# Performance work log

Hardware: AMD Instinct MI355X
Metric: run time of the kernel (lower is better)

Reference implementation:

```python
import jax, jax.numpy as jnp
import numpy as np
import math

EPS = 1e-6          # eps for safe cumprod / clamping
CHUNK = 4           # chunk_size w
SHARP = 1.0         # sharpening_factor
NOISE_STD = 1.0
N_HEADS = 4
ADIM = 512


def moving_sum(x, back, forward):
    """Windowed running sum over last axis: out[k] = sum_{j=k-back}^{k+forward} x[j].
    Equivalent to the conv1d trick in the original (all-ones filter)."""
    k = x.shape[-1]
    pad = [(0, 0)] * (x.ndim - 1) + [(back, forward)]
    c = jnp.cumsum(jnp.pad(x, pad), axis=-1)
    c0 = jnp.concatenate([jnp.zeros_like(c[..., :1]), c], axis=-1)
    w = back + forward
    return c0[..., w + 1: w + 1 + k] - c0[..., :k]


def setup_inputs() -> dict:
    rng = jax.random.key(0)
    ks = jax.random.split(rng, 12)
    B, qlen, klen, kdim, qdim, adim = 8, 256, 2048, 512, 512, ADIM
    s = 0.02
    return {
        "key_enc": jax.random.normal(ks[0], (B, klen, kdim), jnp.float32),
        "query":   jax.random.normal(ks[1], (B, qlen, qdim), jnp.float32),
        "noise":   jax.random.normal(ks[2], (B, qlen, klen), jnp.float32),
        # monotonic energy params
        "Wk_m": jax.random.normal(ks[3], (kdim, adim), jnp.float32) * s,
        "bk_m": jnp.zeros((adim,), jnp.float32),
        "Wq_m": jax.random.normal(ks[4], (qdim, adim), jnp.float32) * s,
        "bq_m": jnp.zeros((adim,), jnp.float32),
        "r":    jnp.array([-4.0], jnp.float32),
        # chunkwise energy params (multi-head)
        "Wk_c": jax.random.normal(ks[5], (kdim, adim), jnp.float32) * s,
        "bk_c": jnp.zeros((adim,), jnp.float32),
        "Wq_c": jax.random.normal(ks[6], (qdim, adim), jnp.float32) * s,
        "bq_c": jnp.zeros((adim,), jnp.float32),
    }


def _mocha_beta(key_enc, query, noise, Wk_m, bk_m, Wq_m, bq_m, r,
                Wk_c, bk_c, Wq_c, bq_c):
    B, klen, _ = key_enc.shape
    qlen = query.shape[1]
    H = N_HEADS
    dk = ADIM // H
    scale = math.sqrt(ADIM)

    # --- monotonic energy (single head): [B, qlen, klen]
    k_m = key_enc @ Wk_m + bk_m
    q_m = query @ Wq_m + bq_m
    e_mono = jnp.einsum('bqa,bka->bqk', q_m, k_m) / scale + r[0]

    # --- p_choose with additive gaussian noise (encourages discreteness)
    p_choose = jax.nn.sigmoid(e_mono + noise * NOISE_STD)  # [B,q,k]

    # --- safe cumprod of (1 - p) via exclusive cumsum in log space
    log1mp = jnp.log(jnp.clip(1.0 - p_choose, EPS, 1.0))
    cumprod_1mp = jnp.exp(jnp.cumsum(log1mp, axis=-1) - log1mp)  # exclusive

    # --- monotonic alpha recurrence over query steps (parallel-mode MoChA)
    aw0 = jnp.zeros((B, klen), jnp.float32).at[:, 0].set(1.0)

    def step(aw_prev, inp):
        p_i, cp_i = inp  # [B, klen]
        alpha_i = p_i * cp_i * jnp.cumsum(
            aw_prev / jnp.clip(cp_i, EPS, 1.0), axis=-1)
        return alpha_i, alpha_i

    xs = (jnp.swapaxes(p_choose, 0, 1), jnp.swapaxes(cumprod_1mp, 0, 1))
    _, alpha_q = jax.lax.scan(step, aw0, xs)          # [q, B, k]
    alpha = jnp.swapaxes(alpha_q, 0, 1)                # [B, q, k]

    # --- chunkwise energy (multi-head): [B, H, q, k]
    k_c = (key_enc @ Wk_c + bk_c).reshape(B, klen, H, dk)
    q_c = (query @ Wq_c + bq_c).reshape(B, qlen, H, dk)
    e_chunk = jnp.einsum('bqhd,bkhd->bhqk', q_c, k_c) / scale

    # --- efficient chunkwise attention (clipped-logit moving-sum softmax)
    e = e_chunk - jnp.max(e_chunk, axis=3, keepdims=True)
    softmax_exp = jnp.maximum(jnp.exp(e), 1e-5)
    denom = moving_sum(softmax_exp, back=CHUNK - 1, forward=0)
    beta = softmax_exp * moving_sum(
        alpha[:, None] * SHARP / denom, back=0, forward=CHUNK - 1)
    return beta  # [B, H, q, k]


def reference(key_enc, query, noise, Wk_m, bk_m, Wq_m, bq_m, r,
              Wk_c, bk_c, Wq_c, bq_c):
    return _mocha_beta(key_enc, query, noise, Wk_m, bk_m, Wq_m, bq_m, r,
                       Wk_c, bk_c, Wq_c, bq_c)
```

## Files before the change

kernel.cpp:

```cpp
#include <hip/hip_runtime.h>
#include <math.h>

#define BATCH   8
#define QLEN    256
#define KLEN    2048
#define KDIM    512
#define NHEADS  4
#define DKH     128
#define NG      5
#define QROWS   (BATCH * QLEN)
#define GCOLS   (NG * 512)

static constexpr float INV_SCALE = 0.04419417382415922f;
static constexpr float EPSV = 1e-6f;

typedef __attribute__((ext_vector_type(8))) short bf16x8;
typedef __attribute__((ext_vector_type(4))) float f32x4;

__device__ __forceinline__ unsigned short f2bf(float f) {
    unsigned u = __builtin_bit_cast(unsigned, f);
    u += 0x7fffu + ((u >> 16) & 1u);
    return (unsigned short)(u >> 16);
}
__device__ __forceinline__ float bf2f(unsigned short u) {
    unsigned x = (unsigned)u << 16;
    return __builtin_bit_cast(float, x);
}

__device__ __forceinline__ void lds_barrier() {
    __asm__ volatile("s_waitcnt lgkmcnt(0)\n\ts_barrier" ::: "memory");
}

__device__ __forceinline__ void gload_lds16(const void* g, void* l) {
    __builtin_amdgcn_global_load_lds(
        (const __attribute__((address_space(1))) void*)g,
        (__attribute__((address_space(3))) void*)l, 16, 0, 0);
}

#define NKXB 8192
#define NQXB 1024
__global__ __launch_bounds__(256) void prep(
    const float* __restrict__ key_enc, const float* __restrict__ query,
    const float* __restrict__ Wk_m, const float* __restrict__ Wk_c,
    const float* __restrict__ Wq_m, const float* __restrict__ Wq_c,
    unsigned short* __restrict__ kx, unsigned short* __restrict__ qx,
    unsigned short* __restrict__ kwm, unsigned short* __restrict__ kwc,
    unsigned short* __restrict__ qwm, unsigned short* __restrict__ qwc)
{
    const int gb = blockIdx.x, tid = threadIdx.x;
    const float* x; unsigned short* y; int i;
    if (gb < NKXB)              { x = key_enc; y = kx; i = gb * 256 + tid; }
    else if (gb < NKXB + NQXB)  { x = query;   y = qx; i = (gb - NKXB) * 256 + tid; }
    else {
        const int w = gb - NKXB - NQXB;
        const int which = w >> 8;
        i = (w & 255) * 256 + tid;
        x = (which == 0) ? Wk_m : (which == 1) ? Wk_c : (which == 2) ? Wq_m : Wq_c;
        y = (which == 0) ? kwm  : (which == 1) ? kwc  : (which == 2) ? qwm  : qwc;
    }
    float4 v = ((const float4*)x)[i];
    ushort4 o;
    o.x = f2bf(v.x); o.y = f2bf(v.y); o.z = f2bf(v.z); o.w = f2bf(v.w);
    ((ushort4*)y)[i] = o;
}

__device__ __forceinline__ void mfma_nt_staged(
    const unsigned short* __restrict__ A, const unsigned short* __restrict__ B,
    int lda, int ldb, int bm, int bn,
    unsigned short* AsLDS, unsigned short* BsLDS, f32x4 acc[4][4], int ksteps)
{
    const int t = threadIdx.x;
    const int wv = t >> 6, ln = t & 63;
    const int r = ln & 15, quad = ln >> 4;
    const int wm = (wv >> 1) * 64, wn = (wv & 1) * 64;
    const int srow = wv * 16 + (ln >> 2);
    const int scol = (ln & 3) * 8;

    for (int ks = 0; ks < ksteps; ++ks) {
        const int k0 = ks * 32;
        #pragma unroll
        for (int j = 0; j < 2; ++j) {
            gload_lds16(A + (size_t)(bm + j * 64 + srow) * lda + k0 + scol,
                        AsLDS + (size_t)(j * 64 + wv * 16) * 32);
            gload_lds16(B + (size_t)(bn + j * 64 + srow) * ldb + k0 + scol,
                        BsLDS + (size_t)(j * 64 + wv * 16) * 32);
        }
        __syncthreads();
        bf16x8 af[4], bg[4];
        #pragma unroll
        for (int f = 0; f < 4; ++f)
            af[f] = *(const bf16x8*)(AsLDS + (size_t)(wm + f * 16 + r) * 32 + quad * 8);
        #pragma unroll
        for (int f = 0; f < 4; ++f)
            bg[f] = *(const bf16x8*)(BsLDS + (size_t)(wn + f * 16 + r) * 32 + quad * 8);
        #pragma unroll
        for (int i = 0; i < 4; ++i)
            #pragma unroll
            for (int j2 = 0; j2 < 4; ++j2)
                acc[i][j2] = __builtin_amdgcn_mfma_f32_16x16x32_bf16(
                    af[i], bg[j2], acc[i][j2], 0, 0, 0);
        __syncthreads();
    }
}

__device__ __forceinline__ void zero_acc(f32x4 acc[4][4]) {
    #pragma unroll
    for (int i = 0; i < 4; ++i)
        #pragma unroll
        for (int j = 0; j < 4; ++j)
            acc[i][j] = f32x4{0.f, 0.f, 0.f, 0.f};
}

__global__ __launch_bounds__(256) void smallg(
    const unsigned short* __restrict__ kwm, const unsigned short* __restrict__ kwc,
    const unsigned short* __restrict__ qwm, const unsigned short* __restrict__ qwc,
    const float* __restrict__ Wk_mf, const float* __restrict__ Wk_cf,
    const float* __restrict__ Wq_mf,
    const float* __restrict__ bq_m, const float* __restrict__ bk_m,
    const float* __restrict__ bq_c,
    unsigned short* __restrict__ GT, float* __restrict__ aux)
{
    __shared__ unsigned short As[128 * 32];
    __shared__ unsigned short Bs[128 * 32];
    __shared__ float red[256];
    const int blk = blockIdx.x, tid = threadIdx.x;

    if (blk < 80) {
        const int seg = blk >> 4, t = blk & 15;
        const int bm = (t >> 2) * 128, bn = (t & 3) * 128;
        const unsigned short *A, *B; int ks;
        if (seg == 0) { A = kwm; B = qwm; ks = 16; }
        else { const int h = seg - 1; A = kwc + h * 128; B = qwc + h * 128; ks = 4; }
        f32x4 acc[4][4]; zero_acc(acc);
        mfma_nt_staged(A, B, 512, 512, bm, bn, As, Bs, acc, ks);
        const int wv = tid >> 6, ln = tid & 63;
        const int r = ln & 15, quad = ln >> 4;
        const int m0 = bm + (wv >> 1) * 64, n0 = bn + (wv & 1) * 64;
        #pragma unroll
        for (int j = 0; j < 4; ++j) {
            const int n = n0 + j * 16 + r;
            #pragma unroll
            for (int i = 0; i < 4; ++i)
                #pragma unroll
                for (int reg = 0; reg < 4; ++reg) {
                    const int m = m0 + i * 16 + quad * 4 + reg;
                    GT[(size_t)(seg * 512 + m) * 512 + n] = f2bf(acc[i][j][reg]);
                }
        }
        return;
    }
    const int ab = blk - 80;
    if (ab < 2) {
        const int d = ab * 256 + tid;
        const float* row = Wk_mf + (size_t)d * 512;
        float s = 0.f;
        for (int j = 0; j < 512; j += 4) {
            float4 a = *(const float4*)(row + j);
            float4 b = *(const float4*)(bq_m + j);
            s += a.x * b.x + a.y * b.y + a.z * b.z + a.w * b.w;
        }
        aux[d] = s; return;
    }
    if (ab < 10) {
        const int t = ab - 2, h = t >> 1;
        const int d = (t & 1) * 256 + tid;
        const float* row = Wk_cf + (size_t)d * 512 + h * 128;
        const float* bv = bq_c + h * 128;
        float s = 0.f;
        for (int j = 0; j < 128; j += 4) {
            float4 a = *(const float4*)(row + j);
            float4 b = *(const float4*)(bv + j);
            s += a.x * b.x + a.y * b.y + a.z * b.z + a.w * b.w;
        }
        aux[512 + h * 512 + d] = s; return;
    }
    if (ab < 12) {
        const int d = (ab - 10) * 256 + tid;
        const float* row = Wq_mf + (size_t)d * 512;
        float s = 0.f;
        for (int j = 0; j < 512; j += 4) {
            float4 a = *(const float4*)(row + j);
            float4 b = *(const float4*)(bk_m + j);
            s += a.x * b.x + a.y * b.y + a.z * b.z + a.w * b.w;
        }
        aux[GCOLS + d] = s; return;
    }
    float s = bq_m[tid] * bk_m[tid] + bq_m[tid + 256] * bk_m[tid + 256];
    red[tid] = s; __syncthreads();
    for (int o = 128; o > 0; o >>= 1) {
        if (tid < o) red[tid] += red[tid + o];
        __syncthreads();
    }
    if (tid == 0) aux[GCOLS + 512] = red[0];
}

__global__ __launch_bounds__(256) void qg_kernel(
    const unsigned short* __restrict__ qx, const unsigned short* __restrict__ GT,
    const float* __restrict__ aux,
    unsigned short* __restrict__ qg, float* __restrict__ vq2)
{
    __shared__ unsigned short As[128 * 32];
    __shared__ unsigned short Bs[128 * 32];
    __shared__ float wuS[512];
    const int v = blockIdx.x, tid = threadIdx.x;
    if (v < 320) {
        const int by = v / 20, bx = v % 20;
        const int bm = by * 128, bn = bx * 128;
        f32x4 acc[4][4]; zero_acc(acc);
        mfma_nt_staged(qx, GT, 512, 512, bm, bn, As, Bs, acc, 16);
        const int wv = tid >> 6, ln = tid & 63;
        const int r = ln & 15, quad = ln >> 4;
        const int m0 = bm + (wv >> 1) * 64, n0 = bn + (wv & 1) * 64;
        #pragma unroll
        for (int j = 0; j < 4; ++j) {
            const int n = n0 + j * 16 + r;
            const float wvb = aux[n];
            #pragma unroll
            for (int i = 0; i < 4; ++i)
                #pragma unroll
                for (int reg = 0; reg < 4; ++reg) {
                    const int m = m0 + i * 16 + quad * 4 + reg;
                    qg[(size_t)m * GCOLS + n] = f2bf(acc[i][j][reg] + wvb);
                }
        }
        return;
    }
    wuS[tid] = aux[GCOLS + tid];
    wuS[tid + 256] = aux[GCOLS + tid + 256];
    __syncthreads();
    const float cc = aux[GCOLS + 512];
    const int q = (v - 320) * 256 + tid;
    const unsigned short* row = qx + (size_t)q * 512;
    float s = 0.f;
    for (int j = 0; j < 512; j += 4) {
        ushort4 a = *(const ushort4*)(row + j);
        s = fmaf(bf2f(a.x), wuS[j], s);
        s = fmaf(bf2f(a.y), wuS[j + 1], s);
        s = fmaf(bf2f(a.z), wuS[j + 2], s);
        s = fmaf(bf2f(a.w), wuS[j + 3], s);
    }
    vq2[q] = (s + cc) * INV_SCALE;
}

__global__ __launch_bounds__(256) void pchoose_mfma(
    const unsigned short* __restrict__ qg, const unsigned short* __restrict__ kx,
    const float* __restrict__ noise, const float* __restrict__ rp,
    const float* __restrict__ vq2, float* __restrict__ p)
{
    __shared__ unsigned short As[128 * 32];
    __shared__ unsigned short Bs[128 * 32];
    const int b = blockIdx.z;
    const unsigned short* A = qg + (size_t)b * QLEN * GCOLS;
    const unsigned short* B = kx + (size_t)b * KLEN * 512;
    const int bm = blockIdx.y * 128, bn = blockIdx.x * 128;
    f32x4 acc[4][4]; zero_acc(acc);
    mfma_nt_staged(A, B, GCOLS, 512, bm, bn, As, Bs, acc, 16);
    const int wv = threadIdx.x >> 6, ln = threadIdx.x & 63;
    const int r = ln & 15, quad = ln >> 4;
    const int m0 = bm + (wv >> 1) * 64, n0 = bn + (wv & 1) * 64;
    const float rv = rp[0];
    #pragma unroll
    for (int i = 0; i < 4; ++i) {
        #pragma unroll
        for (int reg = 0; reg < 4; ++reg) {
            const int q = m0 + i * 16 + quad * 4 + reg;
            const size_t rowoff = ((size_t)b * QLEN + q) * KLEN;
            const float vq = vq2[b * QLEN + q] + rv;
            #pragma unroll
            for (int j = 0; j < 4; ++j) {
                const int k = n0 + j * 16 + r;
                const float e = acc[i][j][reg] * INV_SCALE + vq + noise[rowoff + k];
                p[rowoff + k] = __builtin_amdgcn_rcpf(1.0f + __expf(-e));
            }
        }
    }
}

__device__ __forceinline__ float wave_incl_scan(float x)
{
#define DPP_ADD(ctrl, rmask, bctrl)                                            \
    { int _t = __builtin_amdgcn_update_dpp(0, __builtin_bit_cast(int, x),      \
                                           ctrl, rmask, 0xf, bctrl);           \
      x += __builtin_bit_cast(float, _t); }
    DPP_ADD(0x111, 0xf, true)
    DPP_ADD(0x112, 0xf, true)
    DPP_ADD(0x114, 0xf, true)
    DPP_ADD(0x118, 0xf, true)
    DPP_ADD(0x142, 0xa, false)
    DPP_ADD(0x143, 0xc, false)
#undef DPP_ADD
    return x;
}

__device__ __forceinline__ float row_prefix8(float x)
{
#define DPP_ADD(ctrl)                                                          \
    { int _t = __builtin_amdgcn_update_dpp(0, __builtin_bit_cast(int, x),      \
                                           ctrl, 0xf, 0xf, true);              \
      x += __builtin_bit_cast(float, _t); }
    DPP_ADD(0x111)
    DPP_ADD(0x112)
    DPP_ADD(0x114)
#undef DPP_ADD
    return x;
}

__global__ __launch_bounds__(256) void cumprod_mr(
    const float* __restrict__ p, float* __restrict__ mArr, float* __restrict__ rArr)
{
    const size_t row = blockIdx.x;
    const float* pr = p + row * KLEN;
    float* mr = mArr + row * KLEN;
    float* rr = rArr + row * KLEN;
    const int tid = threadIdx.x;
    const int lane = tid & 63, wid = tid >> 6;
    __shared__ float waveTot[4];

    float4 v0 = *(const float4*)(pr + tid * 8);
    float4 v1 = *(const float4*)(pr + tid * 8 + 4);
    float pv[8] = {v0.x, v0.y, v0.z, v0.w, v1.x, v1.y, v1.z, v1.w};
    float excl[8];
    float run = 0.0f;
    #pragma unroll
    for (int j = 0; j < 8; ++j) {
        float l = __logf(fminf(fmaxf(1.0f - pv[j], EPSV), 1.0f));
        excl[j] = run;
        run += l;
    }
    float s = wave_incl_scan(run);
    if (lane == 63) waveTot[wid] = s;
    __syncthreads();
    float wex = 0.0f;
    for (int w = 0; w < wid; ++w) wex += waveTot[w];
    const float texcl = wex + s - run;

    float mv[8], rv[8];
    #pragma unroll
    for (int j = 0; j < 8; ++j) {
        const float cpv = __expf(texcl + excl[j]);
        mv[j] = pv[j] * cpv;
        rv[j] = __builtin_amdgcn_rcpf(fminf(fmaxf(cpv, EPSV), 1.0f));
    }
    *(float4*)(mr + tid * 8)     = *(float4*)&mv[0];
    *(float4*)(mr + tid * 8 + 4) = *(float4*)&mv[4];
    *(float4*)(rr + tid * 8)     = *(float4*)&rv[0];
    *(float4*)(rr + tid * 8 + 4) = *(float4*)&rv[4];
}

__global__ __launch_bounds__(512, 1) void alpha_echunk(
    const float* __restrict__ mArr, const float* __restrict__ rArr,
    float* __restrict__ alpha,
    const unsigned short* __restrict__ qg, const unsigned short* __restrict__ kx,
    float* __restrict__ out)
{
    __shared__ __align__(16) char smem[98304];
    const int bid = blockIdx.x;
    const int tid = threadIdx.x;

    if (bid < BATCH) {
        __builtin_amdgcn_s_setprio(1);
        float* slots = (float*)smem;
        const int lane = tid & 63, wid = tid >> 6;
        const float* mrow = mArr + (size_t)bid * QLEN * KLEN + tid * 4;
        const float* rrow = rArr + (size_t)bid * QLEN * KLEN + tid * 4;
        float* arow = alpha + (size_t)bid * QLEN * KLEN + tid * 4;

        float aw0 = 0.f, aw1 = 0.f, aw2 = 0.f, aw3 = 0.f;
        if (tid == 0) aw0 = 1.0f;

        float4 mP0 = *(const float4*)(mrow);
        float4 rP0 = *(const float4*)(rrow);
        float4 mP1 = *(const float4*)(mrow + KLEN);
        float4 rP1 = *(const float4*)(rrow + KLEN);
        float4 mQ0 = *(const float4*)(mrow + 2 * (size_t)KLEN);
        float4 rQ0 = *(const float4*)(rrow + 2 * (size_t)KLEN);
        float4 mQ1 = *(const float4*)(mrow + 3 * (size_t)KLEN);
        float4 rQ1 = *(const float4*)(rrow + 3 * (size_t)KLEN);

#define APAIR(I, M0, R0, M1, R1)                                               \
    {                                                                          \
        const int i_ = (I);                               \
        float4 mc0 = M0, rc0 = R0, mc1 = M1, rc1 = R1;                         \
        const int rn_ = (i_ + 4 < QLEN) ? (i_ + 4) : (QLEN - 2);               \
        M0 = *(const float4*)(mrow + (size_t)rn_ * KLEN);                      \
        R0 = *(const float4*)(rrow + (size_t)rn_ * KLEN);                      \
        M1 = *(const float4*)(mrow + (size_t)(rn_ + 1) * KLEN);               \
        R1 = *(const float4*)(rrow + (size_t)(rn_ + 1) * KLEN);               \
                                 \
        float run = 0.f, i0, i1, i2, i3;                                       \
        run = fmaf(aw0, rc0.x, run); i0 = run;                                 \
        run = fmaf(aw1, rc0.y, run); i1 = run;                                 \
        run = fmaf(aw2, rc0.z, run); i2 = run;                                 \
        run = fmaf(aw3, rc0.w, run); i3 = run;                                 \
        const float sx = wave_incl_scan(run);                                  \
        const float wb = sx - run;                                             \
        const float W0 = wb + i0, W1 = wb + i1, W2 = wb + i2, W3 = wb + i3;    \
                      \
        const float u0 = mc0.x * rc1.x, u1 = mc0.y * rc1.y;                    \
        const float u2 = mc0.z * rc1.z, u3 = mc0.w * rc1.w;                    \
        float ur = u0;       const float U0 = ur;                              \
        ur += u1;            const float U1 = ur;                              \
        ur += u2;            const float U2 = ur;                              \
        ur += u3;            const float U3 = ur;                              \
        const float sU = wave_incl_scan(ur);                                   \
        const float ub = sU - ur;                                              \
        float vr = u0 * W0;              const float V0 = vr;                  \
        vr = fmaf(u1, W1, vr);           const float V1 = vr;                  \
        vr = fmaf(u2, W2, vr);           const float V2 = vr;                  \
        vr = fmaf(u3, W3, vr);           const float V3 = vr;                  \
        const float sV = wave_incl_scan(vr);                                   \
        const float vb = sV - vr;                                              \
        const int par = (i_ >> 1) & 1;                                         \
        if (lane == 63) {                                                      \
            float4 tv; tv.x = sx; tv.y = sU; tv.z = sV; tv.w = 0.f;            \
            *(float4*)(slots + (par * 8 + wid) * 4) = tv;                      \
        }                                                                      \
        lds_barrier();                                                         \
        float4 tr = *(const float4*)(slots + (par * 8 + (lane & 7)) * 4);      \
        const float pT = row_prefix8(tr.x);                                    \
        const float Cex = pT - tr.x;                                           \
        const float t2 = fmaf(Cex, tr.y, tr.z);                                \
        const float pQ = row_prefix8(t2);                                      \
        const float C2ex = pQ - t2;                                            \
        const float b0 = __shfl(Cex, wid);                                     \
        const float b1 = __shfl(C2ex, wid);                                    \
                                                          \
        float4 o0;                                                             \
        o0.x = mc0.x * (b0 + W0); o0.y = mc0.y * (b0 + W1);                    \
        o0.z = mc0.z * (b0 + W2); o0.w = mc0.w * (b0 + W3);                    \
        *(float4*)(arow + (size_t)i_ * KLEN) = o0;                             \
                                                        \
        const float X0 = fmaf(b0, ub + U0, vb + V0);                           \
        const float X1 = fmaf(b0, ub + U1, vb + V1);                           \
        const float X2 = fmaf(b0, ub + U2, vb + V2);                           \
        const float X3 = fmaf(b0, ub + U3, vb + V3);                           \
        aw0 = mc1.x * (b1 + X0); aw1 = mc1.y * (b1 + X1);                      \
        aw2 = mc1.z * (b1 + X2); aw3 = mc1.w * (b1 + X3);                      \
        float4 o1; o1.x = aw0; o1.y = aw1; o1.z = aw2; o1.w = aw3;             \
        *(float4*)(arow + (size_t)(i_ + 1) * KLEN) = o1;                       \
    }

        for (int io = 0; io < QLEN; io += 4) {
            APAIR(io + 0, mP0, rP0, mP1, rP1)
            APAIR(io + 2, mQ0, rQ0, mQ1, rQ1)
        }
#undef APAIR
        __builtin_amdgcn_s_setprio(0);
        return;
    }

    const int v = bid - BATCH;
    const int z = v >> 4;
    const int rest = v & 15;
    const int by = rest >> 3;
    const int bx = rest & 7;
    const int b = z >> 2, h = z & 3;
    unsigned short* As = (unsigned short*)smem;
    unsigned short* Bs = (unsigned short*)(smem + 8192);
    const unsigned short* A = qg + (size_t)(b * QLEN) * GCOLS + 512 + h * 512;
    const unsigned short* B = kx + (size_t)b * KLEN * 512;
    const int bm = by * 128, bn = bx * 256;

    const int wv8 = tid >> 6, ln = tid & 63;
    const int r = ln & 15, quad = ln >> 4;
    const int wr = wv8 >> 2, wc = wv8 & 3;
    const int srow = tid >> 2;
    const int scol = (ln & 3) * 8;

    f32x4 acc[4][4]; zero_acc(acc);
    for (int ks = 0; ks < 16; ++ks) {
        const int k0 = ks * 32;
        gload_lds16(A + (size_t)(bm + srow) * GCOLS + k0 + scol,
                    As + (size_t)wv8 * 512);
        gload_lds16(B + (size_t)(bn + srow) * 512 + k0 + scol,
                    Bs + (size_t)wv8 * 512);
        gload_lds16(B + (size_t)(bn + 128 + srow) * 512 + k0 + scol,
                    Bs + 4096 + (size_t)wv8 * 512);
        __syncthreads();
        bf16x8 af[4], bg[4];
        #pragma unroll
        for (int f = 0; f < 4; ++f)
            af[f] = *(const bf16x8*)(As + (size_t)(wr * 64 + f * 16 + r) * 32 + quad * 8);
        #pragma unroll
        for (int f = 0; f < 4; ++f)
            bg[f] = *(const bf16x8*)(Bs + (size_t)(wc * 64 + f * 16 + r) * 32 + quad * 8);
        #pragma unroll
        for (int i = 0; i < 4; ++i)
            #pragma unroll
            for (int j2 = 0; j2 < 4; ++j2)
                acc[i][j2] = __builtin_amdgcn_mfma_f32_16x16x32_bf16(
                    af[i], bg[j2], acc[i][j2], 0, 0, 0);
        __syncthreads();
    }
    {
        const int m0 = bm + wr * 64, n0 = bn + wc * 64;
        #pragma unroll
        for (int i = 0; i < 4; ++i) {
            #pragma unroll
            for (int reg = 0; reg < 4; ++reg) {
                const int q = m0 + i * 16 + quad * 4 + reg;
                const size_t rowoff = ((size_t)z * QLEN + q) * KLEN;
                #pragma unroll
                for (int j = 0; j < 4; ++j) {
                    const int k = n0 + j * 16 + r;
                    out[rowoff + k] = acc[i][j][reg] * INV_SCALE;
                }
            }
        }
    }
}

__global__ __launch_bounds__(256) void beta_kernel(
    float* __restrict__ eo, const float* __restrict__ alpha)
{
    __shared__ float sse[KLEN + 3];
    __shared__ float su[KLEN + 3];
    __shared__ float wmax[4];

    const int tid = threadIdx.x;
    const int lane = tid & 63, wid = tid >> 6;
    const int row = blockIdx.x;
    const int q = row & (QLEN - 1);
    const int b = row >> 10;
    float* erow = eo + (size_t)row * KLEN;
    const float* arow = alpha + ((size_t)b * QLEN + q) * KLEN;

    if (tid < 3) { sse[tid] = 0.0f; su[KLEN + tid] = 0.0f; }

    float ev[8];
    float lm = -INFINITY;
    #pragma unroll
    for (int j = 0; j < 8; ++j) {
        const int k = tid + 256 * j;
        ev[j] = erow[k];
        lm = fmaxf(lm, ev[j]);
    }
    #pragma unroll
    for (int off = 32; off > 0; off >>= 1) lm = fmaxf(lm, __shfl_xor(lm, off));
    if (lane == 0) wmax[wid] = lm;
    __syncthreads();
    const float mx = fmaxf(fmaxf(wmax[0], wmax[1]), fmaxf(wmax[2], wmax[3]));

    #pragma unroll
    for (int j = 0; j < 8; ++j) {
        const int k = tid + 256 * j;
        sse[k + 3] = fmaxf(__expf(ev[j] - mx), 1e-5f);
    }
    __syncthreads();

    #pragma unroll
    for (int j = 0; j < 8; ++j) {
        const int k = tid + 256 * j;
        const float denom = sse[k + 3] + sse[k + 2] + sse[k + 1] + sse[k];
        su[k] = arow[k] * __builtin_amdgcn_rcpf(denom);
    }
    __syncthreads();

    #pragma unroll
    for (int j = 0; j < 8; ++j) {
        const int k = tid + 256 * j;
        erow[k] = sse[k + 3] * (su[k] + su[k + 1] + su[k + 2] + su[k + 3]);
    }
}

extern "C" void kernel_launch(void* const* d_in, const int* in_sizes, int n_in,
                              void* d_out, int out_size, void* d_ws, size_t ws_size,
                              hipStream_t stream)
{
    (void)in_sizes; (void)n_in; (void)out_size; (void)ws_size;
    const float* key_enc = (const float*)d_in[0];
    const float* query   = (const float*)d_in[1];
    const float* noise   = (const float*)d_in[2];
    const float* Wk_m    = (const float*)d_in[3];
    const float* bk_m    = (const float*)d_in[4];
    const float* Wq_m    = (const float*)d_in[5];
    const float* bq_m    = (const float*)d_in[6];
    const float* rp      = (const float*)d_in[7];
    const float* Wk_c    = (const float*)d_in[8];
    const float* bk_c    = (const float*)d_in[9];
    const float* Wq_c    = (const float*)d_in[10];
    const float* bq_c    = (const float*)d_in[11];
    float* out = (float*)d_out;
    (void)bk_c;

    char* w = (char*)d_ws;
    unsigned short* kx   = (unsigned short*)w; w += (size_t)BATCH * KLEN * KDIM * 2;
    unsigned short* qx   = (unsigned short*)w; w += (size_t)QROWS * KDIM * 2;
    unsigned short* kwm  = (unsigned short*)w; w += (size_t)512 * 512 * 2;
    unsigned short* kwc  = (unsigned short*)w; w += (size_t)512 * 512 * 2;
    unsigned short* qwm  = (unsigned short*)w; w += (size_t)512 * 512 * 2;
    unsigned short* qwc  = (unsigned short*)w; w += (size_t)512 * 512 * 2;
    unsigned short* GT   = (unsigned short*)w; w += (size_t)GCOLS * 512 * 2;
    unsigned short* qg   = (unsigned short*)w; w += (size_t)QROWS * GCOLS * 2;
    float* aux    = (float*)w; w += 4096 * 4;
    float* vq2    = (float*)w; w += QROWS * 4;
    float* p_alpha = (float*)w; w += (size_t)BATCH * QLEN * KLEN * 4;
    float* mArr    = (float*)w; w += (size_t)BATCH * QLEN * KLEN * 4;
    float* rArr    = (float*)w;

    hipLaunchKernelGGL(prep, dim3(NKXB + NQXB + 1024), dim3(256), 0, stream,
                       key_enc, query, Wk_m, Wk_c, Wq_m, Wq_c,
                       kx, qx, kwm, kwc, qwm, qwc);

    hipLaunchKernelGGL(smallg, dim3(93), dim3(256), 0, stream,
                       kwm, kwc, qwm, qwc, Wk_m, Wk_c, Wq_m,
                       bq_m, bk_m, bq_c, GT, aux);

    hipLaunchKernelGGL(qg_kernel, dim3(328), dim3(256), 0, stream,
                       qx, GT, aux, qg, vq2);

    hipLaunchKernelGGL(pchoose_mfma, dim3(KLEN / 128, QLEN / 128, BATCH), dim3(256), 0, stream,
                       qg, kx, noise, rp, vq2, p_alpha);

    hipLaunchKernelGGL(cumprod_mr, dim3(BATCH * QLEN), dim3(256), 0, stream,
                       p_alpha, mArr, rArr);

    hipLaunchKernelGGL(alpha_echunk, dim3(BATCH + 512), dim3(512), 0, stream,
                       mArr, rArr, p_alpha, qg, kx, out);

    hipLaunchKernelGGL(beta_kernel, dim3(BATCH * NHEADS * QLEN), dim3(256), 0, stream,
                       out, p_alpha);
}
```

Baseline: 279.2 us.

## Fuse cumprod into alpha scan and merge weight prep into GEMM kernel

Removes the separate cumprod_mr kernel. The alpha recurrence kernel now computes the safe cumprod (m and 1/cp) for upcoming rows inline from p, which drops the write and re-read of two full BxQxK float arrays. It also folds the weight bf16 conversion into the small Gram GEMM by converting fp32 on the fly, and merges prep and smallg into a single launch. The cost is more serial work and extra cross-wave reductions inside the latency-bound scan loop.

```diff
diff --git a/kernel.cpp b/kernel.cpp
--- a/kernel.cpp
+++ b/kernel.cpp
@@ -37,33 +37,6 @@
         (__attribute__((address_space(3))) void*)l, 16, 0, 0);
 }
 
-#define NKXB 8192
-#define NQXB 1024
-__global__ __launch_bounds__(256) void prep(
-    const float* __restrict__ key_enc, const float* __restrict__ query,
-    const float* __restrict__ Wk_m, const float* __restrict__ Wk_c,
-    const float* __restrict__ Wq_m, const float* __restrict__ Wq_c,
-    unsigned short* __restrict__ kx, unsigned short* __restrict__ qx,
-    unsigned short* __restrict__ kwm, unsigned short* __restrict__ kwc,
-    unsigned short* __restrict__ qwm, unsigned short* __restrict__ qwc)
-{
-    const int gb = blockIdx.x, tid = threadIdx.x;
-    const float* x; unsigned short* y; int i;
-    if (gb < NKXB)              { x = key_enc; y = kx; i = gb * 256 + tid; }
-    else if (gb < NKXB + NQXB)  { x = query;   y = qx; i = (gb - NKXB) * 256 + tid; }
-    else {
-        const int w = gb - NKXB - NQXB;
-        const int which = w >> 8;
-        i = (w & 255) * 256 + tid;
-        x = (which == 0) ? Wk_m : (which == 1) ? Wk_c : (which == 2) ? Wq_m : Wq_c;
-        y = (which == 0) ? kwm  : (which == 1) ? kwc  : (which == 2) ? qwm  : qwc;
-    }
-    float4 v = ((const float4*)x)[i];
-    ushort4 o;
-    o.x = f2bf(v.x); o.y = f2bf(v.y); o.z = f2bf(v.z); o.w = f2bf(v.w);
-    ((ushort4*)y)[i] = o;
-}
-
 __device__ __forceinline__ void mfma_nt_staged(
     const unsigned short* __restrict__ A, const unsigned short* __restrict__ B,
     int lda, int ldb, int bm, int bn,
@@ -103,6 +76,57 @@
     }
 }
 
+__device__ __forceinline__ void mfma_nt_staged_f32(
+    const float* __restrict__ A, const float* __restrict__ B,
+    int lda, int ldb, int bm, int bn,
+    unsigned short* AsLDS, unsigned short* BsLDS, f32x4 acc[4][4], int ksteps)
+{
+    const int t = threadIdx.x;
+    const int wv = t >> 6, ln = t & 63;
+    const int r = ln & 15, quad = ln >> 4;
+    const int wm = (wv >> 1) * 64, wn = (wv & 1) * 64;
+    const int srow = wv * 16 + (ln >> 2);
+    const int scol = (ln & 3) * 8;
+
+    for (int ks = 0; ks < ksteps; ++ks) {
+        const int k0 = ks * 32;
+        #pragma unroll
+        for (int j = 0; j < 2; ++j) {
+            const float* ap = A + (size_t)(bm + j * 64 + srow) * lda + k0 + scol;
+            float4 a0 = *(const float4*)ap, a1 = *(const float4*)(ap + 4);
+            bf16x8 av;
+            av[0] = (short)f2bf(a0.x); av[1] = (short)f2bf(a0.y);
+            av[2] = (short)f2bf(a0.z); av[3] = (short)f2bf(a0.w);
+            av[4] = (short)f2bf(a1.x); av[5] = (short)f2bf(a1.y);
+            av[6] = (short)f2bf(a1.z); av[7] = (short)f2bf(a1.w);
+            *(bf16x8*)(AsLDS + (size_t)(j * 64 + wv * 16) * 32 + ln * 8) = av;
+            const float* bp = B + (size_t)(bn + j * 64 + srow) * ldb + k0 + scol;
+            float4 b0 = *(const float4*)bp, b1 = *(const float4*)(bp + 4);
+            bf16x8 bv;
+            bv[0] = (short)f2bf(b0.x); bv[1] = (short)f2bf(b0.y);
+            bv[2] = (short)f2bf(b0.z); bv[3] = (short)f2bf(b0.w);
+            bv[4] = (short)f2bf(b1.x); bv[5] = (short)f2bf(b1.y);
+            bv[6] = (short)f2bf(b1.z); bv[7] = (short)f2bf(b1.w);
+            *(bf16x8*)(BsLDS + (size_t)(j * 64 + wv * 16) * 32 + ln * 8) = bv;
+        }
+        __syncthreads();
+        bf16x8 af[4], bg[4];
+        #pragma unroll
+        for (int f = 0; f < 4; ++f)
+            af[f] = *(const bf16x8*)(AsLDS + (size_t)(wm + f * 16 + r) * 32 + quad * 8);
+        #pragma unroll
+        for (int f = 0; f < 4; ++f)
+            bg[f] = *(const bf16x8*)(BsLDS + (size_t)(wn + f * 16 + r) * 32 + quad * 8);
+        #pragma unroll
+        for (int i = 0; i < 4; ++i)
+            #pragma unroll
+            for (int j2 = 0; j2 < 4; ++j2)
+                acc[i][j2] = __builtin_amdgcn_mfma_f32_16x16x32_bf16(
+                    af[i], bg[j2], acc[i][j2], 0, 0, 0);
+        __syncthreads();
+    }
+}
+
 __device__ __forceinline__ void zero_acc(f32x4 acc[4][4]) {
     #pragma unroll
     for (int i = 0; i < 4; ++i)
@@ -111,28 +135,41 @@
             acc[i][j] = f32x4{0.f, 0.f, 0.f, 0.f};
 }
 
-__global__ __launch_bounds__(256) void smallg(
-    const unsigned short* __restrict__ kwm, const unsigned short* __restrict__ kwc,
-    const unsigned short* __restrict__ qwm, const unsigned short* __restrict__ qwc,
-    const float* __restrict__ Wk_mf, const float* __restrict__ Wk_cf,
-    const float* __restrict__ Wq_mf,
+#define NKXB 8192
+#define NQXB 1024
+__global__ __launch_bounds__(256) void prep_g(
+    const float* __restrict__ key_enc, const float* __restrict__ query,
+    const float* __restrict__ Wk_m, const float* __restrict__ Wk_c,
+    const float* __restrict__ Wq_m, const float* __restrict__ Wq_c,
     const float* __restrict__ bq_m, const float* __restrict__ bk_m,
     const float* __restrict__ bq_c,
+    unsigned short* __restrict__ kx, unsigned short* __restrict__ qx,
     unsigned short* __restrict__ GT, float* __restrict__ aux)
 {
     __shared__ unsigned short As[128 * 32];
     __shared__ unsigned short Bs[128 * 32];
     __shared__ float red[256];
-    const int blk = blockIdx.x, tid = threadIdx.x;
-
-    if (blk < 80) {
-        const int seg = blk >> 4, t = blk & 15;
-        const int bm = (t >> 2) * 128, bn = (t & 3) * 128;
-        const unsigned short *A, *B; int ks;
-        if (seg == 0) { A = kwm; B = qwm; ks = 16; }
-        else { const int h = seg - 1; A = kwc + h * 128; B = qwc + h * 128; ks = 4; }
+    const int gb = blockIdx.x, tid = threadIdx.x;
+
+    if (gb < NKXB + NQXB) {
+        const float* x = (gb < NKXB) ? key_enc : query;
+        unsigned short* y = (gb < NKXB) ? kx : qx;
+        const int i = (gb < NKXB ? gb : gb - NKXB) * 256 + tid;
+        float4 v = ((const float4*)x)[i];
+        ushort4 o;
+        o.x = f2bf(v.x); o.y = f2bf(v.y); o.z = f2bf(v.z); o.w = f2bf(v.w);
+        ((ushort4*)y)[i] = o;
+        return;
+    }
+    const int t = gb - NKXB - NQXB;
+    if (t < 80) {
+        const int seg = t >> 4, tt = t & 15;
+        const int bm = (tt >> 2) * 128, bn = (tt & 3) * 128;
+        const float *A, *B; int ks;
+        if (seg == 0) { A = Wk_m; B = Wq_m; ks = 16; }
+        else { const int h = seg - 1; A = Wk_c + h * 128; B = Wq_c + h * 128; ks = 4; }
         f32x4 acc[4][4]; zero_acc(acc);
-        mfma_nt_staged(A, B, 512, 512, bm, bn, As, Bs, acc, ks);
+        mfma_nt_staged_f32(A, B, 512, 512, bm, bn, As, Bs, acc, ks);
         const int wv = tid >> 6, ln = tid & 63;
         const int r = ln & 15, quad = ln >> 4;
         const int m0 = bm + (wv >> 1) * 64, n0 = bn + (wv & 1) * 64;
@@ -149,10 +186,10 @@
         }
         return;
     }
-    const int ab = blk - 80;
+    const int ab = t - 80;
     if (ab < 2) {
         const int d = ab * 256 + tid;
-        const float* row = Wk_mf + (size_t)d * 512;
+        const float* row = Wk_m + (size_t)d * 512;
         float s = 0.f;
         for (int j = 0; j < 512; j += 4) {
             float4 a = *(const float4*)(row + j);
@@ -162,9 +199,9 @@
         aux[d] = s; return;
     }
     if (ab < 10) {
-        const int t = ab - 2, h = t >> 1;
-        const int d = (t & 1) * 256 + tid;
-        const float* row = Wk_cf + (size_t)d * 512 + h * 128;
+        const int tt = ab - 2, h = tt >> 1;
+        const int d = (tt & 1) * 256 + tid;
+        const float* row = Wk_c + (size_t)d * 512 + h * 128;
         const float* bv = bq_c + h * 128;
         float s = 0.f;
         for (int j = 0; j < 128; j += 4) {
@@ -176,7 +213,7 @@
     }
     if (ab < 12) {
         const int d = (ab - 10) * 256 + tid;
-        const float* row = Wq_mf + (size_t)d * 512;
+        const float* row = Wq_m + (size_t)d * 512;
         float s = 0.f;
         for (int j = 0; j < 512; j += 4) {
             float4 a = *(const float4*)(row + j);
@@ -305,51 +342,35 @@
     return x;
 }
 
-__global__ __launch_bounds__(256) void cumprod_mr(
-    const float* __restrict__ p, float* __restrict__ mArr, float* __restrict__ rArr)
-{
-    const size_t row = blockIdx.x;
-    const float* pr = p + row * KLEN;
-    float* mr = mArr + row * KLEN;
-    float* rr = rArr + row * KLEN;
-    const int tid = threadIdx.x;
-    const int lane = tid & 63, wid = tid >> 6;
-    __shared__ float waveTot[4];
-
-    float4 v0 = *(const float4*)(pr + tid * 8);
-    float4 v1 = *(const float4*)(pr + tid * 8 + 4);
-    float pv[8] = {v0.x, v0.y, v0.z, v0.w, v1.x, v1.y, v1.z, v1.w};
-    float excl[8];
-    float run = 0.0f;
-    #pragma unroll
-    for (int j = 0; j < 8; ++j) {
-        float l = __logf(fminf(fmaxf(1.0f - pv[j], EPSV), 1.0f));
-        excl[j] = run;
-        run += l;
-    }
-    float s = wave_incl_scan(run);
-    if (lane == 63) waveTot[wid] = s;
-    __syncthreads();
-    float wex = 0.0f;
-    for (int w = 0; w < wid; ++w) wex += waveTot[w];
-    const float texcl = wex + s - run;
-
-    float mv[8], rv[8];
-    #pragma unroll
-    for (int j = 0; j < 8; ++j) {
-        const float cpv = __expf(texcl + excl[j]);
-        mv[j] = pv[j] * cpv;
-        rv[j] = __builtin_amdgcn_rcpf(fminf(fmaxf(cpv, EPSV), 1.0f));
-    }
-    *(float4*)(mr + tid * 8)     = *(float4*)&mv[0];
-    *(float4*)(mr + tid * 8 + 4) = *(float4*)&mv[4];
-    *(float4*)(rr + tid * 8)     = *(float4*)&rv[0];
-    *(float4*)(rr + tid * 8 + 4) = *(float4*)&rv[4];
-}
+#define CUMPREP(PV, TP, STOT)                                                  \
+    {                                                                          \
+        const float l0_ = __logf(fminf(fmaxf(1.0f - (PV).x, EPSV), 1.0f));     \
+        const float l1_ = __logf(fminf(fmaxf(1.0f - (PV).y, EPSV), 1.0f));     \
+        const float l2_ = __logf(fminf(fmaxf(1.0f - (PV).z, EPSV), 1.0f));     \
+        const float l3_ = __logf(fminf(fmaxf(1.0f - (PV).w, EPSV), 1.0f));     \
+        const float e1_ = l0_, e2_ = l0_ + l1_, e3_ = e2_ + l2_;               \
+        const float run_ = e3_ + l3_;                                          \
+        STOT = wave_incl_scan(run_);                                           \
+        const float wb_ = STOT - run_;                                         \
+        (TP).x = wb_; (TP).y = wb_ + e1_; (TP).z = wb_ + e2_;                  \
+        (TP).w = wb_ + e3_;                                                    \
+    }
+#define CUMFIN(PV, TP, WEX, M, R)                                              \
+    {                                                                          \
+        const float c0_ = __expf((WEX) + (TP).x);                              \
+        const float c1_ = __expf((WEX) + (TP).y);                              \
+        const float c2_ = __expf((WEX) + (TP).z);                              \
+        const float c3_ = __expf((WEX) + (TP).w);                              \
+        (M).x = (PV).x * c0_; (M).y = (PV).y * c1_;                            \
+        (M).z = (PV).z * c2_; (M).w = (PV).w * c3_;                            \
+        (R).x = __builtin_amdgcn_rcpf(fminf(fmaxf(c0_, EPSV), 1.0f));          \
+        (R).y = __builtin_amdgcn_rcpf(fminf(fmaxf(c1_, EPSV), 1.0f));          \
+        (R).z = __builtin_amdgcn_rcpf(fminf(fmaxf(c2_, EPSV), 1.0f));          \
+        (R).w = __builtin_amdgcn_rcpf(fminf(fmaxf(c3_, EPSV), 1.0f));          \
+    }
 
 __global__ __launch_bounds__(512, 1) void alpha_echunk(
-    const float* __restrict__ mArr, const float* __restrict__ rArr,
-    float* __restrict__ alpha,
+    float* pa,
     const unsigned short* __restrict__ qg, const unsigned short* __restrict__ kx,
     float* __restrict__ out)
 {
@@ -359,45 +380,61 @@
 
     if (bid < BATCH) {
         __builtin_amdgcn_s_setprio(1);
-        float* slots = (float*)smem;
+        float (*slots)[4] = (float (*)[4])smem;
+        float* slotsB = (float*)(smem + 256);
         const int lane = tid & 63, wid = tid >> 6;
-        const float* mrow = mArr + (size_t)bid * QLEN * KLEN + tid * 4;
-        const float* rrow = rArr + (size_t)bid * QLEN * KLEN + tid * 4;
-        float* arow = alpha + (size_t)bid * QLEN * KLEN + tid * 4;
+        float* prow = pa + (size_t)bid * QLEN * KLEN + tid * 4;
 
         float aw0 = 0.f, aw1 = 0.f, aw2 = 0.f, aw3 = 0.f;
         if (tid == 0) aw0 = 1.0f;
 
-        float4 mP0 = *(const float4*)(mrow);
-        float4 rP0 = *(const float4*)(rrow);
-        float4 mP1 = *(const float4*)(mrow + KLEN);
-        float4 rP1 = *(const float4*)(rrow + KLEN);
-        float4 mQ0 = *(const float4*)(mrow + 2 * (size_t)KLEN);
-        float4 rQ0 = *(const float4*)(rrow + 2 * (size_t)KLEN);
-        float4 mQ1 = *(const float4*)(mrow + 3 * (size_t)KLEN);
-        float4 rQ1 = *(const float4*)(rrow + 3 * (size_t)KLEN);
-
-#define APAIR(I, M0, R0, M1, R1)                                               \
+        float4 mA0, rA0, mA1, rA1, mB0, rB0, mB1, rB1;
+        float4 pCa, pCb, pNa, pNb;
+
+        {
+            float4 p0 = *(const float4*)(prow);
+            float4 p1 = *(const float4*)(prow + KLEN);
+            pCa = *(const float4*)(prow + 2 * (size_t)KLEN);
+            pCb = *(const float4*)(prow + 3 * (size_t)KLEN);
+            pNa = *(const float4*)(prow + 4 * (size_t)KLEN);
+            pNb = *(const float4*)(prow + 5 * (size_t)KLEN);
+            float4 tp0, tp1; float s0, s1;
+            CUMPREP(p0, tp0, s0)
+            CUMPREP(p1, tp1, s1)
+            if (lane == 63) {
+                float4 tv; tv.x = s0; tv.y = s1; tv.z = 0.f; tv.w = 0.f;
+                *(float4*)(slots[8 + wid]) = tv;
+            }
+            lds_barrier();
+            float4 tr = *(const float4*)(slots[8 + (lane & 7)]);
+            const float px0 = row_prefix8(tr.x); const float e0x = px0 - tr.x;
+            const float px1 = row_prefix8(tr.y); const float e1x = px1 - tr.y;
+            const float wex0 = __shfl(e0x, wid);
+            const float wex1 = __shfl(e1x, wid);
+            CUMFIN(p0, tp0, wex0, mA0, rA0)
+            CUMFIN(p1, tp1, wex1, mA1, rA1)
+        }
+
+#define APAIR(I, MC0, RC0, MC1, RC1, MN0, RN0, MN1, RN1)                       \
     {                                                                          \
         const int i_ = (I);                               \
-        float4 mc0 = M0, rc0 = R0, mc1 = M1, rc1 = R1;                         \
-        const int rn_ = (i_ + 4 < QLEN) ? (i_ + 4) : (QLEN - 2);               \
-        M0 = *(const float4*)(mrow + (size_t)rn_ * KLEN);                      \
-        R0 = *(const float4*)(rrow + (size_t)rn_ * KLEN);                      \
-        M1 = *(const float4*)(mrow + (size_t)(rn_ + 1) * KLEN);               \
-        R1 = *(const float4*)(rrow + (size_t)(rn_ + 1) * KLEN);               \
+        const int par_ = (i_ >> 1) & 1;                                        \
+                  \
+        float4 tpa_, tpb_; float sa_, sb_;                                     \
+        CUMPREP(pCa, tpa_, sa_)                                                \
+        CUMPREP(pCb, tpb_, sb_)                                                \
                                  \
         float run = 0.f, i0, i1, i2, i3;                                       \
-        run = fmaf(aw0, rc0.x, run); i0 = run;                                 \
-        run = fmaf(aw1, rc0.y, run); i1 = run;                                 \
-        run = fmaf(aw2, rc0.z, run); i2 = run;                                 \
-        run = fmaf(aw3, rc0.w, run); i3 = run;                                 \
+        run = fmaf(aw0, RC0.x, run); i0 = run;                                 \
+        run = fmaf(aw1, RC0.y, run); i1 = run;                                 \
+        run = fmaf(aw2, RC0.z, run); i2 = run;                                 \
+        run = fmaf(aw3, RC0.w, run); i3 = run;                                 \
         const float sx = wave_incl_scan(run);                                  \
         const float wb = sx - run;                                             \
         const float W0 = wb + i0, W1 = wb + i1, W2 = wb + i2, W3 = wb + i3;    \
                       \
-        const float u0 = mc0.x * rc1.x, u1 = mc0.y * rc1.y;                    \
-        const float u2 = mc0.z * rc1.z, u3 = mc0.w * rc1.w;                    \
+        const float u0 = MC0.x * RC1.x, u1 = MC0.y * RC1.y;                    \
+        const float u2 = MC0.z * RC1.z, u3 = MC0.w * RC1.w;                    \
         float ur = u0;       const float U0 = ur;                              \
         ur += u1;            const float U1 = ur;                              \
         ur += u2;            const float U2 = ur;                              \
@@ -410,39 +447,57 @@
         vr = fmaf(u3, W3, vr);           const float V3 = vr;                  \
         const float sV = wave_incl_scan(vr);                                   \
         const float vb = sV - vr;                                              \
-        const int par = (i_ >> 1) & 1;                                         \
         if (lane == 63) {                                                      \
-            float4 tv; tv.x = sx; tv.y = sU; tv.z = sV; tv.w = 0.f;            \
-            *(float4*)(slots + (par * 8 + wid) * 4) = tv;                      \
+            float4 tv; tv.x = sx; tv.y = sU; tv.z = sV; tv.w = sa_;            \
+            *(float4*)(slots[par_ * 8 + wid]) = tv;                            \
+            slotsB[par_ * 8 + wid] = sb_;                                      \
         }                                                                      \
         lds_barrier();                                                         \
-        float4 tr = *(const float4*)(slots + (par * 8 + (lane & 7)) * 4);      \
+        float4 tr = *(const float4*)(slots[par_ * 8 + (lane & 7)]);            \
+        const float trB = slotsB[par_ * 8 + (lane & 7)];                       \
         const float pT = row_prefix8(tr.x);                                    \
         const float Cex = pT - tr.x;                                           \
         const float t2 = fmaf(Cex, tr.y, tr.z);                                \
         const float pQ = row_prefix8(t2);                                      \
         const float C2ex = pQ - t2;                                            \
+        float tw_ = tr.w;                                                      \
+        const float pLa = row_prefix8(tw_);                                    \
+        const float Laex = pLa - tr.w;                                         \
+        float tb_ = trB;                                                       \
+        const float pLb = row_prefix8(tb_);                                    \
+        const float Lbex = pLb - trB;                                          \
         const float b0 = __shfl(Cex, wid);                                     \
         const float b1 = __shfl(C2ex, wid);                                    \
-                                                          \
+        const float wexa = __shfl(Laex, wid);                                  \
+        const float wexb = __shfl(Lbex, wid);                                  \
+                              \
         float4 o0;                                                             \
-        o0.x = mc0.x * (b0 + W0); o0.y = mc0.y * (b0 + W1);                    \
-        o0.z = mc0.z * (b0 + W2); o0.w = mc0.w * (b0 + W3);                    \
-        *(float4*)(arow + (size_t)i_ * KLEN) = o0;                             \
+        o0.x = MC0.x * (b0 + W0); o0.y = MC0.y * (b0 + W1);                    \
+        o0.z = MC0.z * (b0 + W2); o0.w = MC0.w * (b0 + W3);                    \
+        *(float4*)(prow + (size_t)i_ * KLEN) = o0;                             \
                                                         \
         const float X0 = fmaf(b0, ub + U0, vb + V0);                           \
         const float X1 = fmaf(b0, ub + U1, vb + V1);                           \
         const float X2 = fmaf(b0, ub + U2, vb + V2);                           \
         const float X3 = fmaf(b0, ub + U3, vb + V3);                           \
-        aw0 = mc1.x * (b1 + X0); aw1 = mc1.y * (b1 + X1);                      \
-        aw2 = mc1.z * (b1 + X2); aw3 = mc1.w * (b1 + X3);                      \
+        aw0 = MC1.x * (b1 + X0); aw1 = MC1.y * (b1 + X1);                      \
+        aw2 = MC1.z * (b1 + X2); aw3 = MC1.w * (b1 + X3);                      \
         float4 o1; o1.x = aw0; o1.y = aw1; o1.z = aw2; o1.w = aw3;             \
-        *(float4*)(arow + (size_t)(i_ + 1) * KLEN) = o1;                       \
+        *(float4*)(prow + (size_t)(i_ + 1) * KLEN) = o1;                       \
+                        \
+        CUMFIN(pCa, tpa_, wexa, MN0, RN0)                                      \
+        CUMFIN(pCb, tpb_, wexb, MN1, RN1)                                      \
+                                 \
+        pCa = pNa; pCb = pNb;                                                  \
+        const int rla_ = (i_ + 6 < QLEN) ? (i_ + 6) : (QLEN - 1);              \
+        const int rlb_ = (i_ + 7 < QLEN) ? (i_ + 7) : (QLEN - 1);              \
+        pNa = *(const float4*)(prow + (size_t)rla_ * KLEN);                    \
+        pNb = *(const float4*)(prow + (size_t)rlb_ * KLEN);                    \
     }
 
         for (int io = 0; io < QLEN; io += 4) {
-            APAIR(io + 0, mP0, rP0, mP1, rP1)
-            APAIR(io + 2, mQ0, rQ0, mQ1, rQ1)
+            APAIR(io + 0, mA0, rA0, mA1, rA1, mB0, rB0, mB1, rB1)
+            APAIR(io + 2, mB0, rB0, mB1, rB1, mA0, rA0, mA1, rA1)
         }
 #undef APAIR
         __builtin_amdgcn_s_setprio(0);
@@ -586,25 +641,15 @@
     char* w = (char*)d_ws;
     unsigned short* kx   = (unsigned short*)w; w += (size_t)BATCH * KLEN * KDIM * 2;
     unsigned short* qx   = (unsigned short*)w; w += (size_t)QROWS * KDIM * 2;
-    unsigned short* kwm  = (unsigned short*)w; w += (size_t)512 * 512 * 2;
-    unsigned short* kwc  = (unsigned short*)w; w += (size_t)512 * 512 * 2;
-    unsigned short* qwm  = (unsigned short*)w; w += (size_t)512 * 512 * 2;
-    unsigned short* qwc  = (unsigned short*)w; w += (size_t)512 * 512 * 2;
     unsigned short* GT   = (unsigned short*)w; w += (size_t)GCOLS * 512 * 2;
     unsigned short* qg   = (unsigned short*)w; w += (size_t)QROWS * GCOLS * 2;
     float* aux    = (float*)w; w += 4096 * 4;
     float* vq2    = (float*)w; w += QROWS * 4;
-    float* p_alpha = (float*)w; w += (size_t)BATCH * QLEN * KLEN * 4;
-    float* mArr    = (float*)w; w += (size_t)BATCH * QLEN * KLEN * 4;
-    float* rArr    = (float*)w;
-
-    hipLaunchKernelGGL(prep, dim3(NKXB + NQXB + 1024), dim3(256), 0, stream,
+    float* p_alpha = (float*)w;
+
+    hipLaunchKernelGGL(prep_g, dim3(NKXB + NQXB + 93), dim3(256), 0, stream,
                        key_enc, query, Wk_m, Wk_c, Wq_m, Wq_c,
-                       kx, qx, kwm, kwc, qwm, qwc);
-
-    hipLaunchKernelGGL(smallg, dim3(93), dim3(256), 0, stream,
-                       kwm, kwc, qwm, qwc, Wk_m, Wk_c, Wq_m,
-                       bq_m, bk_m, bq_c, GT, aux);
+                       bq_m, bk_m, bq_c, kx, qx, GT, aux);
 
     hipLaunchKernelGGL(qg_kernel, dim3(328), dim3(256), 0, stream,
                        qx, GT, aux, qg, vq2);
@@ -612,11 +657,8 @@
     hipLaunchKernelGGL(pchoose_mfma, dim3(KLEN / 128, QLEN / 128, BATCH), dim3(256), 0, stream,
                        qg, kx, noise, rp, vq2, p_alpha);
 
-    hipLaunchKernelGGL(cumprod_mr, dim3(BATCH * QLEN), dim3(256), 0, stream,
-                       p_alpha, mArr, rArr);
-
     hipLaunchKernelGGL(alpha_echunk, dim3(BATCH + 512), dim3(512), 0, stream,
-                       mArr, rArr, p_alpha, qg, kx, out);
+                       p_alpha, qg, kx, out);
 
     hipLaunchKernelGGL(beta_kernel, dim3(BATCH * NHEADS * QLEN), dim3(256), 0, stream,
                        out, p_alpha);
```

Result: slower. 355.7 us (+27.4%).
